# Optimization experiments

Hardware: AMD Instinct MI355X
Metric: run time of the kernel (lower is better)

## Reference

```python
import jax, jax.numpy as jnp
import numpy as np

N, C, E, NUM_ID, NUM_LABELS = 50000, 128, 1600000, 2048, 7


def setup_inputs() -> dict:
    key = jax.random.key(0)
    k_x, k_r, k_c, k_id, k_lab, k_w, k_wid = jax.random.split(key, 7)
    x = jax.random.normal(k_x, (N, C), dtype=jnp.float32)
    row = jax.random.randint(k_r, (E,), 0, N)
    col = jax.random.randint(k_c, (E,), 0, N)
    # remove accidental self-loops so the 'add remaining self loops' step
    # (append all N self loops) matches PyG's add_remaining_self_loops exactly
    col = jnp.where(col == row, (col + 1) % N, col)
    edge_index = jnp.stack([row, col]).astype(jnp.int64)
    idx = jax.random.randint(k_id, (NUM_ID,), 0, N).astype(jnp.int64)
    node_label = jax.random.randint(k_lab, (N,), 0, 8).astype(jnp.int64)
    # glorot init
    s = jnp.sqrt(6.0 / (C + C)).astype(jnp.float32)
    weight = jax.random.uniform(k_w, (C, C), minval=-s, maxval=s, dtype=jnp.float32)
    weight_id = jax.random.uniform(k_wid, (NUM_LABELS, C, C), minval=-s, maxval=s, dtype=jnp.float32)
    return {"x": x, "edge_index": edge_index, "id": idx, "node_label": node_label,
            "weight": weight, "weight_id": weight_id}


def reference(x, edge_index, id, node_label, weight, weight_id):
    n = x.shape[0]
    row, col = edge_index[0], edge_index[1]
    # ego-center update: x[id] += x[id] @ W (index_add handles duplicate ids)
    x = x.at[id].add(x[id] @ weight)
    # label-grouped gather-matmul-scatter: ox = x + sum_i mask_i * (x @ W_i)
    ox = x
    for i in range(NUM_LABELS):
        mask = (node_label == i + 1)
        ox = ox + jnp.where(mask[:, None], x @ weight_id[i], jnp.zeros((), x.dtype))
    # GCN symmetric normalization with self loops (fill_value = 1.0)
    loop = jnp.arange(n)
    row_f = jnp.concatenate([row, loop])
    col_f = jnp.concatenate([col, loop])
    ew = jnp.ones((row_f.shape[0],), dtype=x.dtype)
    deg = jax.ops.segment_sum(ew, row_f, num_segments=n)
    dinv = jnp.where(deg > 0, deg ** -0.5, jnp.zeros((), x.dtype))
    norm = dinv[row_f] * ew * dinv[col_f]
    # message = norm * x_j (source row), aggregated by sum at target col
    out = jax.ops.segment_sum(norm[:, None] * ox[row_f], col_f, num_segments=n)
    return out
```

## Files before the change

### kernel.cpp

```cpp
#include <hip/hip_runtime.h>
#include <hip/hip_bf16.h>

typedef unsigned int   u32;
typedef unsigned short u16;
typedef unsigned char  u8;
typedef float f32x2 __attribute__((ext_vector_type(2)));

#define N_NODES 50000
#define C_DIM   128
#define E_EDGES 1600000
#define NUM_IDX 2048

#define CPB 256
#define NB  196
#define CHK 4096
#define NP  391
#define PT  512
#define NLB 98
#define GB  16

__global__ __launch_bounds__(PT) void hist_all_kernel(
        const int* __restrict__ row, const int* __restrict__ col,
        int* __restrict__ Hc, int* __restrict__ Hr,
        const int* __restrict__ label, int* __restrict__ labCnt,
        const int* __restrict__ id, int* __restrict__ cnt) {
    int t = threadIdx.x;
    if (blockIdx.x >= NP) {
        __shared__ int h[8];
        if (t < 8) h[t] = 0;
        __syncthreads();
        int n = (blockIdx.x - NP) * PT + t;
        if (n < N_NODES) atomicAdd(&h[label[n]], 1);
        if (n < NUM_IDX) atomicAdd(&cnt[id[n]], 1);
        __syncthreads();
        if (t < 8 && h[t] > 0) atomicAdd(&labCnt[t], h[t]);
        return;
    }
    __shared__ int hc[NB], hr[NB];
    int p = blockIdx.x;
    for (int i = t; i < NB; i += PT) { hc[i] = 0; hr[i] = 0; }
    __syncthreads();
    int e0 = p * CHK, e1 = min(e0 + CHK, E_EDGES);
    for (int e = e0 + t; e < e1; e += PT) {
        atomicAdd(&hc[col[e] >> 8], 1);
        atomicAdd(&hr[row[e] >> 8], 1);
    }
    __syncthreads();
    for (int i = t; i < NB; i += PT) {
        Hc[p * NB + i] = hc[i];
        Hr[p * NB + i] = hr[i];
    }
}

__global__ __launch_bounds__(PT) void offsets_kernel(
        int* __restrict__ Hc, int* __restrict__ Hr,
        int* __restrict__ colTot, int* __restrict__ rowTot) {
    __shared__ int sc[PT];
    int b = blockIdx.x;
    int j = (b < NB) ? b : b - NB;
    int* H   = (b < NB) ? Hc : Hr;
    int* tot = (b < NB) ? colTot : rowTot;
    int t = threadIdx.x;
    int v = (t < NP) ? H[t * NB + j] : 0;
    sc[t] = v;
    __syncthreads();
    for (int off = 1; off < PT; off <<= 1) {
        int a = (t >= off) ? sc[t - off] : 0;
        int s = sc[t];
        __syncthreads();
        sc[t] = s + a;
        __syncthreads();
    }
    if (t < NP) H[t * NB + j] = sc[t] - v;
    if (t == PT - 1) tot[j] = sc[t];
}

__global__ void bucket_scan_kernel(const int* __restrict__ colTot, const int* __restrict__ rowTot,
                                   int* __restrict__ bucketStart, int* __restrict__ rowStart,
                                   const int* __restrict__ labCnt, int* __restrict__ labCur) {
    __shared__ int sc[256];
    int t = threadIdx.x;
    sc[t] = (t < NB) ? colTot[t] : 0;
    __syncthreads();
    for (int off = 1; off < 256; off <<= 1) {
        int v = sc[t];
        int a = (t >= off) ? sc[t - off] : 0;
        __syncthreads();
        sc[t] = v + a;
        __syncthreads();
    }
    if (t < NB) {
        bucketStart[t] = (t == 0) ? 0 : sc[t - 1];
        if (t == NB - 1) bucketStart[NB] = sc[t];
    }
    __syncthreads();
    sc[t] = (t < NB) ? rowTot[t] : 0;
    __syncthreads();
    for (int off = 1; off < 256; off <<= 1) {
        int v = sc[t];
        int a = (t >= off) ? sc[t - off] : 0;
        __syncthreads();
        sc[t] = v + a;
        __syncthreads();
    }
    if (t < NB) {
        rowStart[t] = (t == 0) ? 0 : sc[t - 1];
        if (t == NB - 1) rowStart[NB] = sc[t];
    }
    if (t == 0) {
        int run = 0;
        for (int i = 0; i < 8; ++i) { labCur[i] = run; run += labCnt[i]; }
    }
}

__global__ __launch_bounds__(PT) void part_fill_kernel(
        const int* __restrict__ row, const int* __restrict__ col,
        const int* __restrict__ Hc, const int* __restrict__ Hr,
        const int* __restrict__ bucketStart, const int* __restrict__ rowStart,
        u32* __restrict__ S, u8* __restrict__ Sr,
        const int* __restrict__ label, int* __restrict__ labCur,
        int* __restrict__ nodeByLabel) {
    int t = threadIdx.x;
    if (blockIdx.x >= NP) {
        __shared__ int h8[8], base8[8], c28[8];
        if (t < 8) { h8[t] = 0; c28[t] = 0; }
        __syncthreads();
        int n = (blockIdx.x - NP) * PT + t;
        int l = 0;
        if (n < N_NODES) { l = label[n]; atomicAdd(&h8[l], 1); }
        __syncthreads();
        if (t < 8 && h8[t] > 0) base8[t] = atomicAdd(&labCur[t], h8[t]);
        __syncthreads();
        if (n < N_NODES) {
            int pos = base8[l] + atomicAdd(&c28[l], 1);
            nodeByLabel[pos] = n;
        }
        return;
    }
    __shared__ int bc_[NB], br_[NB];
    int p = blockIdx.x;
    for (int i = t; i < NB; i += PT) {
        bc_[i] = bucketStart[i] + Hc[p * NB + i];
        br_[i] = rowStart[i]   + Hr[p * NB + i];
    }
    __syncthreads();
    int e0 = p * CHK, e1 = min(e0 + CHK, E_EDGES);
    for (int e = e0 + t; e < e1; e += PT) {
        int r = row[e], c = col[e];
        int pc = atomicAdd(&bc_[c >> 8], 1);
        S[pc] = ((u32)r << 8) | (u32)(c & 255);
        int pr = atomicAdd(&br_[r >> 8], 1);
        Sr[pr] = (u8)(r & 255);
    }
}

__global__ __launch_bounds__(PT) void csr_deg_kernel(
        const u32* __restrict__ S, const u8* __restrict__ Sr,
        const int* __restrict__ bucketStart, const int* __restrict__ rowStart,
        int* __restrict__ start, u16* __restrict__ srcrow,
        float* __restrict__ dinv) {
    __shared__ int h[CPB], cur[CPB], sc[CPB];
    int t = threadIdx.x;
    if (blockIdx.x >= NB) {
        int b = blockIdx.x - NB;
        if (t < CPB) h[t] = 0;
        __syncthreads();
        int e0 = rowStart[b], e1 = rowStart[b + 1];
        for (int e = e0 + t; e < e1; e += PT) atomicAdd(&h[Sr[e]], 1);
        __syncthreads();
        if (t < CPB) {
            int n = b * CPB + t;
            if (n < N_NODES) dinv[n] = rsqrtf((float)(h[t] + 1));
        }
        return;
    }
    int b = blockIdx.x;
    if (t < CPB) h[t] = 0;
    __syncthreads();
    int e0 = bucketStart[b], e1 = bucketStart[b + 1];
    for (int e = e0 + t; e < e1; e += PT) atomicAdd(&h[S[e] & 255u], 1);
    __syncthreads();
    if (t < CPB) sc[t] = h[t];
    __syncthreads();
    for (int off = 1; off < CPB; off <<= 1) {
        int v = 0, a = 0;
        if (t < CPB) { v = sc[t]; a = (t >= off) ? sc[t - off] : 0; }
        __syncthreads();
        if (t < CPB) sc[t] = v + a;
        __syncthreads();
    }
    if (t < CPB) {
        int base = (t == 0) ? 0 : sc[t - 1];
        int gcol = b * CPB + t;
        if (gcol < N_NODES) start[gcol] = e0 + base;
        cur[t] = base;
    }
    if (b == NB - 1 && t == 0) start[N_NODES] = E_EDGES;
    __syncthreads();
    for (int e = e0 + t; e < e1; e += PT) {
        u32 v = S[e];
        int pos = atomicAdd(&cur[v & 255u], 1);
        srcrow[e0 + pos] = (u16)(v >> 8);
    }
}

__global__ void node_msg_kernel(const float* __restrict__ x,
                                const int* __restrict__ cnt,
                                const int* __restrict__ label,
                                const float* __restrict__ dinv,
                                const float* __restrict__ W,
                                const float* __restrict__ Wid,
                                const int* __restrict__ nodeByLabel,
                                __hip_bfloat16* __restrict__ msgb) {
    __shared__ float xs[GB][C_DIM];
    __shared__ int nid[GB], lab[GB], cc[GB];
    int t = threadIdx.x;
    if (t < GB) {
        int n = nodeByLabel[blockIdx.x * GB + t];
        nid[t] = n; lab[t] = label[n]; cc[t] = cnt[n];
    }
    __syncthreads();
    #pragma unroll
    for (int g = 0; g < GB; ++g)
        xs[g][t] = __builtin_nontemporal_load(x + (size_t)nid[g] * C_DIM + t);
    __syncthreads();
    for (int g = 0; g < GB; ++g) {
        int c = cc[g];
        if (c > 0) {
            float acc = 0.f;
            #pragma unroll 8
            for (int k = 0; k < C_DIM; ++k) acc += xs[g][k] * W[k * C_DIM + t];
            __syncthreads();
            xs[g][t] += (float)c * acc;
            __syncthreads();
        }
    }
    float res[GB];
    #pragma unroll
    for (int g = 0; g < GB; ++g) res[g] = xs[g][t];
    if (lab[0] == lab[GB - 1]) {
        int L = lab[0];
        if (L > 0) {
            const float* Wl = Wid + (size_t)(L - 1) * C_DIM * C_DIM;
            float acc[GB];
            #pragma unroll
            for (int g = 0; g < GB; ++g) acc[g] = 0.f;
            for (int k = 0; k < C_DIM; ++k) {
                float w = Wl[k * C_DIM + t];
                #pragma unroll
                for (int g = 0; g < GB; ++g) acc[g] += xs[g][k] * w;
            }
            #pragma unroll
            for (int g = 0; g < GB; ++g) res[g] += acc[g];
        }
    } else {
        for (int g = 0; g < GB; ++g) {
            int L = lab[g];
            if (L > 0) {
                const float* Wl = Wid + (size_t)(L - 1) * C_DIM * C_DIM;
                float acc = 0.f;
                #pragma unroll 8
                for (int k = 0; k < C_DIM; ++k) acc += xs[g][k] * Wl[k * C_DIM + t];
                res[g] += acc;
            }
        }
    }
    #pragma unroll
    for (int g = 0; g < GB; ++g) {
        int n = nid[g];
        msgb[(size_t)n * C_DIM + t] = __float2bfloat16(dinv[n] * res[g]);
    }
}

__global__ void gather_kernel(const int* __restrict__ start,
                              const u16* __restrict__ srcrow,
                              const float* __restrict__ dinv,
                              const u32* __restrict__ m32,
                              float* __restrict__ out) {
    int wid  = threadIdx.x >> 6;
    int lane = threadIdx.x & 63;
    int c = blockIdx.x * 4 + wid;
    int e0 = start[c], e1 = start[c + 1];
    u32 u = m32[((u32)c << 6) | lane];
    float a0 = __uint_as_float(u << 16);
    float a1 = __uint_as_float(u & 0xffff0000u);
    int e = e0;
    for (; e + 8 <= e1; e += 8) {
        u32 rr[8], uu[8];
        #pragma unroll
        for (int j = 0; j < 8; ++j) rr[j] = srcrow[e + j];
        #pragma unroll
        for (int j = 0; j < 8; ++j) uu[j] = m32[(rr[j] << 6) | (u32)lane];
        #pragma unroll
        for (int j = 0; j < 8; ++j) {
            a0 += __uint_as_float(uu[j] << 16);
            a1 += __uint_as_float(uu[j] & 0xffff0000u);
        }
    }
    for (; e < e1; ++e) {
        u32 ue = m32[((u32)srcrow[e] << 6) | (u32)lane];
        a0 += __uint_as_float(ue << 16);
        a1 += __uint_as_float(ue & 0xffff0000u);
    }
    float di = dinv[c];
    f32x2 o; o.x = di * a0; o.y = di * a1;
    __builtin_nontemporal_store(o, (f32x2*)out + (((u32)c << 6) | lane));
}

extern "C" void kernel_launch(void* const* d_in, const int* in_sizes, int n_in,
                              void* d_out, int out_size, void* d_ws, size_t ws_size,
                              hipStream_t stream) {
    const float* x     = (const float*)d_in[0];
    const int*   edge  = (const int*)d_in[1];
    const int*   id    = (const int*)d_in[2];
    const int*   label = (const int*)d_in[3];
    const float* W     = (const float*)d_in[4];
    const float* Wid   = (const float*)d_in[5];
    float*       out   = (float*)d_out;

    const int* row = edge;
    const int* col = edge + E_EDGES;

    __hip_bfloat16* msgb = (__hip_bfloat16*)d_ws;
    u32* S           = (u32*)(msgb + (size_t)N_NODES * C_DIM);
    u16* srcrow      = (u16*)(S + E_EDGES);
    u8*  Sr          = (u8*)(srcrow + E_EDGES);
    int* start       = (int*)(Sr + E_EDGES);
    int* bucketStart = start + (N_NODES + 1);
    int* rowStart    = bucketStart + (NB + 1);
    int* Hc          = rowStart + (NB + 1);
    int* Hr          = Hc + NP * NB;
    int* colTot      = Hr + NP * NB;
    int* rowTot      = colTot + NB;
    int* nodeByLabel = rowTot + NB;
    float* dinv      = (float*)(nodeByLabel + N_NODES);
    int* cnt         = (int*)(dinv + N_NODES);
    int* labCnt      = cnt + N_NODES;
    int* labCur      = labCnt + 8;

    hipMemsetAsync(cnt, 0, ((size_t)N_NODES + 16) * sizeof(int), stream);

    hist_all_kernel   <<<NP + NLB, PT, 0, stream>>>(row, col, Hc, Hr,
                                                    label, labCnt, id, cnt);
    offsets_kernel    <<<2 * NB, PT, 0, stream>>>(Hc, Hr, colTot, rowTot);
    bucket_scan_kernel<<<1, 256, 0, stream>>>(colTot, rowTot, bucketStart, rowStart,
                                              labCnt, labCur);
    part_fill_kernel  <<<NP + NLB, PT, 0, stream>>>(row, col, Hc, Hr, bucketStart, rowStart,
                                                    S, Sr, label, labCur, nodeByLabel);
    csr_deg_kernel    <<<2 * NB, PT, 0, stream>>>(S, Sr, bucketStart, rowStart,
                                                  start, srcrow, dinv);
    node_msg_kernel   <<<N_NODES / GB, C_DIM, 0, stream>>>(x, cnt, label, dinv, W, Wid,
                                                           nodeByLabel, msgb);
    gather_kernel     <<<N_NODES / 4, 256, 0, stream>>>(start, srcrow, dinv,
                                                        (const u32*)msgb, out);
}
```

Measured before the change: 252.4 us.

## Stage label weights in LDS and double node batch per block in node_msg

The node message kernel now handles 32 label-sorted nodes per 256-thread block instead of 16 nodes per 128 threads. For uniform-label blocks, the label weight matrix is staged into shared memory in two 64-row halves, and each half-block computes 16 nodes with float4 x reads. This reuses each weight load across twice as many nodes and vectorizes the x gather. In exchange it uses about 48KB of LDS per block, which may cut occupancy, and the mixed-label and ego-update paths run redundantly across both halves.

```diff
diff --git a/kernel.cpp b/kernel.cpp
--- a/kernel.cpp
+++ b/kernel.cpp
@@ -17,7 +17,8 @@
 #define NP  391
 #define PT  512
 #define NLB 98
-#define GB  16
+#define NBLK 32
+#define NMB ((N_NODES + NBLK - 1) / NBLK)
 
 __global__ __launch_bounds__(PT) void hist_all_kernel(
         const int* __restrict__ row, const int* __restrict__ col,
@@ -204,71 +205,108 @@
     }
 }
 
-__global__ void node_msg_kernel(const float* __restrict__ x,
-                                const int* __restrict__ cnt,
-                                const int* __restrict__ label,
-                                const float* __restrict__ dinv,
-                                const float* __restrict__ W,
-                                const float* __restrict__ Wid,
-                                const int* __restrict__ nodeByLabel,
-                                __hip_bfloat16* __restrict__ msgb) {
-    __shared__ float xs[GB][C_DIM];
-    __shared__ int nid[GB], lab[GB], cc[GB];
-    int t = threadIdx.x;
-    if (t < GB) {
-        int n = nodeByLabel[blockIdx.x * GB + t];
+__global__ __launch_bounds__(256) void node_msg_kernel(
+        const float* __restrict__ x, const int* __restrict__ cnt,
+        const int* __restrict__ label, const float* __restrict__ dinv,
+        const float* __restrict__ W, const float* __restrict__ Wid,
+        const int* __restrict__ nodeByLabel, __hip_bfloat16* __restrict__ msgb) {
+    __shared__ float Wl[64 * C_DIM];
+    __shared__ float xs[NBLK * C_DIM];
+    __shared__ int nid[NBLK], lab[NBLK], cc[NBLK];
+    int t = threadIdx.x;
+    int s = t >> 7, c = t & 127;
+    int base = blockIdx.x * NBLK;
+    int nb = min(NBLK, N_NODES - base);
+    if (t < nb) {
+        int n = nodeByLabel[base + t];
         nid[t] = n; lab[t] = label[n]; cc[t] = cnt[n];
     }
     __syncthreads();
-    #pragma unroll
-    for (int g = 0; g < GB; ++g)
-        xs[g][t] = __builtin_nontemporal_load(x + (size_t)nid[g] * C_DIM + t);
-    __syncthreads();
-    for (int g = 0; g < GB; ++g) {
-        int c = cc[g];
-        if (c > 0) {
+    for (int idx = t; idx < nb * 32; idx += 256) {
+        int g = idx >> 5, c4 = (idx & 31) << 2;
+        *(float4*)&xs[g * C_DIM + c4] =
+            *(const float4*)&x[(size_t)nid[g] * C_DIM + c4];
+    }
+    __syncthreads();
+    for (int g = 0; g < nb; ++g) {
+        int cg = cc[g];
+        if (cg > 0) {
             float acc = 0.f;
             #pragma unroll 8
-            for (int k = 0; k < C_DIM; ++k) acc += xs[g][k] * W[k * C_DIM + t];
+            for (int k = 0; k < C_DIM; ++k)
+                acc += xs[g * C_DIM + k] * W[k * C_DIM + c];
             __syncthreads();
-            xs[g][t] += (float)c * acc;
+            if (s == 0) xs[g * C_DIM + c] += (float)cg * acc;
             __syncthreads();
         }
     }
-    float res[GB];
-    #pragma unroll
-    for (int g = 0; g < GB; ++g) res[g] = xs[g][t];
-    if (lab[0] == lab[GB - 1]) {
-        int L = lab[0];
-        if (L > 0) {
-            const float* Wl = Wid + (size_t)(L - 1) * C_DIM * C_DIM;
-            float acc[GB];
+    int L0 = lab[0], L1 = lab[nb - 1];
+    if (L0 == L1 && L0 > 0) {
+        const float* Wg = Wid + (size_t)(L0 - 1) * C_DIM * C_DIM;
+        float acc[16];
+        #pragma unroll
+        for (int g = 0; g < 16; ++g) acc[g] = 0.f;
+        int gbase = s * 16;
+        int gcnt = nb - gbase; if (gcnt < 0) gcnt = 0; if (gcnt > 16) gcnt = 16;
+        for (int i = t; i < 64 * 32; i += 256) {
+            int kk = i >> 5, c4 = (i & 31) << 2;
+            *(float4*)&Wl[kk * C_DIM + c4] = *(const float4*)&Wg[kk * C_DIM + c4];
+        }
+        __syncthreads();
+        for (int k = 0; k < 64; k += 4) {
+            float w0 = Wl[k * C_DIM + c],       w1 = Wl[(k + 1) * C_DIM + c];
+            float w2 = Wl[(k + 2) * C_DIM + c], w3 = Wl[(k + 3) * C_DIM + c];
             #pragma unroll
-            for (int g = 0; g < GB; ++g) acc[g] = 0.f;
-            for (int k = 0; k < C_DIM; ++k) {
-                float w = Wl[k * C_DIM + t];
-                #pragma unroll
-                for (int g = 0; g < GB; ++g) acc[g] += xs[g][k] * w;
+            for (int g = 0; g < 16; ++g) {
+                float4 xv = *(const float4*)&xs[(gbase + g) * C_DIM + k];
+                acc[g] += w0 * xv.x + w1 * xv.y + w2 * xv.z + w3 * xv.w;
             }
+        }
+        __syncthreads();
+        for (int i = t; i < 64 * 32; i += 256) {
+            int kk = i >> 5, c4 = (i & 31) << 2;
+            *(float4*)&Wl[kk * C_DIM + c4] = *(const float4*)&Wg[(64 + kk) * C_DIM + c4];
+        }
+        __syncthreads();
+        for (int k = 0; k < 64; k += 4) {
+            float w0 = Wl[k * C_DIM + c],       w1 = Wl[(k + 1) * C_DIM + c];
+            float w2 = Wl[(k + 2) * C_DIM + c], w3 = Wl[(k + 3) * C_DIM + c];
             #pragma unroll
-            for (int g = 0; g < GB; ++g) res[g] += acc[g];
+            for (int g = 0; g < 16; ++g) {
+                float4 xv = *(const float4*)&xs[(gbase + g) * C_DIM + 64 + k];
+                acc[g] += w0 * xv.x + w1 * xv.y + w2 * xv.z + w3 * xv.w;
+            }
+        }
+        for (int g = 0; g < gcnt; ++g) {
+            int n = nid[gbase + g];
+            msgb[(size_t)n * C_DIM + c] =
+                __float2bfloat16(dinv[n] * (xs[(gbase + g) * C_DIM + c] + acc[g]));
+        }
+    } else if (L0 == L1) {
+        int gbase = s * 16;
+        int gcnt = nb - gbase; if (gcnt < 0) gcnt = 0; if (gcnt > 16) gcnt = 16;
+        for (int g = 0; g < gcnt; ++g) {
+            int n = nid[gbase + g];
+            msgb[(size_t)n * C_DIM + c] =
+                __float2bfloat16(dinv[n] * xs[(gbase + g) * C_DIM + c]);
         }
     } else {
-        for (int g = 0; g < GB; ++g) {
+        for (int g = 0; g < nb; ++g) {
             int L = lab[g];
+            float res = xs[g * C_DIM + c];
             if (L > 0) {
-                const float* Wl = Wid + (size_t)(L - 1) * C_DIM * C_DIM;
+                const float* Wg = Wid + (size_t)(L - 1) * C_DIM * C_DIM;
                 float acc = 0.f;
                 #pragma unroll 8
-                for (int k = 0; k < C_DIM; ++k) acc += xs[g][k] * Wl[k * C_DIM + t];
-                res[g] += acc;
+                for (int k = 0; k < C_DIM; ++k)
+                    acc += xs[g * C_DIM + k] * Wg[k * C_DIM + c];
+                res += acc;
             }
-        }
-    }
-    #pragma unroll
-    for (int g = 0; g < GB; ++g) {
-        int n = nid[g];
-        msgb[(size_t)n * C_DIM + t] = __float2bfloat16(dinv[n] * res[g]);
+            if (s == 0) {
+                int n = nid[g];
+                msgb[(size_t)n * C_DIM + c] = __float2bfloat16(dinv[n] * res);
+            }
+        }
     }
 }
 
@@ -349,8 +387,8 @@
                                                     S, Sr, label, labCur, nodeByLabel);
     csr_deg_kernel    <<<2 * NB, PT, 0, stream>>>(S, Sr, bucketStart, rowStart,
                                                   start, srcrow, dinv);
-    node_msg_kernel   <<<N_NODES / GB, C_DIM, 0, stream>>>(x, cnt, label, dinv, W, Wid,
-                                                           nodeByLabel, msgb);
+    node_msg_kernel   <<<NMB, 256, 0, stream>>>(x, cnt, label, dinv, W, Wid,
+                                                nodeByLabel, msgb);
     gather_kernel     <<<N_NODES / 4, 256, 0, stream>>>(start, srcrow, dinv,
                                                         (const u32*)msgb, out);
 }
```

New measurement: 304.7 us. 20.7% more time.
